# Kernel optimization log

Measured on AMD Instinct MI355X. Metric: run time of the kernel, lower is better.

The kernel has to match this reference:

```python
import jax, jax.numpy as jnp
import numpy as np

EPS = 1e-5
B, D_ENT, D_REL = 1024, 400, 400
OUT, KW = 32, 9
N_ENT = 50000


def _bn(x, g, b, axes):
    # batch-norm with batch statistics (training-mode math), eps=1e-5
    mu = jnp.mean(x, axis=axes, keepdims=True)
    var = jnp.var(x, axis=axes, keepdims=True)
    return (x - mu) * jax.lax.rsqrt(var + EPS) * g + b


def setup_inputs() -> dict:
    key = jax.random.key(0)
    ks = jax.random.split(key, 6)
    return {
        "e1_emb": jax.random.normal(ks[0], (B, D_ENT), jnp.float32),
        "rel_emb": jax.random.normal(ks[1], (B, D_REL), jnp.float32),
        "all_ent_w": jax.random.normal(ks[2], (N_ENT, D_ENT), jnp.float32),
        "fc1_w": jax.random.normal(ks[3], (OUT * KW, D_REL), jnp.float32) * 0.05,
        "fc1_b": jnp.zeros((OUT * KW,), jnp.float32),
        "fc_w": jax.random.normal(ks[4], (D_ENT, (D_ENT - KW + 1) * OUT), jnp.float32) * 0.02,
        "fc_b": jnp.zeros((D_ENT,), jnp.float32),
        "bn0_g": jnp.ones((1,), jnp.float32),
        "bn0_b": jnp.zeros((1,), jnp.float32),
        "bn1_g": jnp.ones((OUT,), jnp.float32),
        "bn1_b": jnp.zeros((OUT,), jnp.float32),
        "bn2_g": jnp.ones((D_ENT,), jnp.float32),
        "bn2_b": jnp.zeros((D_ENT,), jnp.float32),
    }


def reference(e1_emb, rel_emb, all_ent_w, fc1_w, fc1_b, fc_w, fc_b,
              bn0_g, bn0_b, bn1_g, bn1_b, bn2_g, bn2_b):
    d = e1_emb.shape[1]
    L = d - KW + 1  # conv output width (kernel_h=1, in_channels=1)

    # bn0: BatchNorm2d(1) over view [B,1,1,d] -> stats over all elements
    x = _bn(e1_emb, bn0_g, bn0_b, axes=(0, 1))  # [B, d]

    # hypernetwork: relation -> per-sample conv kernels [B, OUT, KW]
    k = (rel_emb @ fc1_w.T + fc1_b).reshape(-1, OUT, KW)

    # per-sample 1x9 conv (groups=B) as windows + batched contraction
    # xw[b, l, w] = x[b, l + w]
    xw = jnp.stack([x[:, w:w + L] for w in range(KW)], axis=-1)  # [B, L, KW]
    conv = jnp.einsum('blw,bow->bol', xw, k)  # [B, OUT, L]

    # bn1: BatchNorm2d(OUT), per-channel stats over (batch, width)
    h = _bn(conv, bn1_g[None, :, None], bn1_b[None, :, None], axes=(0, 2))

    # flatten channel-major (matches torch .view(B, -1) on [B, OUT, 1, L])
    h = h.reshape(h.shape[0], OUT * L)
    h = h @ fc_w.T + fc_b  # [B, d]

    # bn2: BatchNorm1d(d), per-feature stats over batch
    h = jax.nn.relu(_bn(h, bn2_g, bn2_b, axes=(0,)))

    return h @ all_ent_w.T  # [B, N_ENT]
```

## Files before the change

kernel.cpp:

```cpp
#include <hip/hip_runtime.h>
#include <stdint.h>

typedef unsigned short u16;
typedef short bf16x8 __attribute__((ext_vector_type(8)));
typedef float f32x4 __attribute__((ext_vector_type(4)));
typedef u16 u16x4 __attribute__((ext_vector_type(4)));
typedef u16 u16x8 __attribute__((ext_vector_type(8)));

#define B_SZ   1024
#define D_IN   400
#define L_OUT  392
#define OC     32
#define KW     9
#define K_FC   12544
#define N_ENT  50000
#define NPAD_ENT 50048
#define KPAD_H 448
#define NPAD_FC 512
#define SPLIT_FC 14

__device__ __forceinline__ u16 f2bf(float f) {
  uint32_t u = __builtin_bit_cast(uint32_t, f);
  u += 0x7FFFu + ((u >> 16) & 1u);
  return (u16)(u >> 16);
}
__device__ __forceinline__ float bf2f(u16 v) {
  uint32_t u = ((uint32_t)v) << 16;
  return __builtin_bit_cast(float, u);
}

__device__ __forceinline__ void gload_lds16(const u16* g, u16* l) {
  __builtin_amdgcn_global_load_lds(
      (const __attribute__((address_space(1))) unsigned int*)g,
      (__attribute__((address_space(3))) unsigned int*)l, 16, 0, 0);
}

__device__ __forceinline__ void block_reduce2(float& s1, float& s2, float* sm) {
  for (int d = 32; d; d >>= 1) { s1 += __shfl_down(s1, d); s2 += __shfl_down(s2, d); }
  int wave = threadIdx.x >> 6, lane = threadIdx.x & 63;
  if (lane == 0) { sm[wave * 2] = s1; sm[wave * 2 + 1] = s2; }
  __syncthreads();
  if (threadIdx.x == 0) {
    s1 = sm[0] + sm[2] + sm[4] + sm[6];
    s2 = sm[1] + sm[3] + sm[5] + sm[7];
  }
}

__global__ __launch_bounds__(256) void red0(const float* __restrict__ e1, float* __restrict__ part0) {
  int t = threadIdx.x;
  int idx = blockIdx.x * 256 + t;
  float s1 = 0.f, s2 = 0.f;
  for (int i = idx; i < B_SZ * D_IN; i += 256 * 256) { float v = e1[i]; s1 += v; s2 += v * v; }
  __shared__ float sm[8];
  block_reduce2(s1, s2, sm);
  if (t == 0) { part0[blockIdx.x * 2] = s1; part0[blockIdx.x * 2 + 1] = s2; }
}

__global__ __launch_bounds__(256) void comb0(const float* __restrict__ part0,
                                             const float* __restrict__ g0,
                                             const float* __restrict__ b0,
                                             float* __restrict__ stats) {
  int t = threadIdx.x;
  float s1 = part0[t * 2], s2 = part0[t * 2 + 1];
  __shared__ float sm[8];
  block_reduce2(s1, s2, sm);
  if (t == 0) {
    const float N = (float)(B_SZ * D_IN);
    float mu = s1 / N, var = s2 / N - mu * mu;
    float a = g0[0] * rsqrtf(var + 1e-5f);
    stats[0] = a;
    stats[1] = b0[0] - mu * a;
  }
}

__global__ __launch_bounds__(256) void fc1_gemm(const float* __restrict__ rel,
                                                const float* __restrict__ W,
                                                const float* __restrict__ bias,
                                                float* __restrict__ outk) {
  __shared__ __align__(16) float As[16 * 68];
  __shared__ __align__(16) float Bs[16 * 68];
  int mt = blockIdx.x, nt = blockIdx.y;
  int t = threadIdx.x;
  int tx = t & 15, ty = t >> 4;
  int lr = t >> 2, lk = (t & 3) * 4;
  float acc[4][4] = {};
  for (int k0 = 0; k0 < 400; k0 += 16) {
    __syncthreads();
    float4 av = *(const float4*)(rel + (size_t)(mt * 64 + lr) * 400 + k0 + lk);
    int brow = nt * 64 + lr;
    float4 bv = {0.f, 0.f, 0.f, 0.f};
    if (brow < 288) bv = *(const float4*)(W + (size_t)brow * 400 + k0 + lk);
    As[(lk + 0) * 68 + lr] = av.x; As[(lk + 1) * 68 + lr] = av.y;
    As[(lk + 2) * 68 + lr] = av.z; As[(lk + 3) * 68 + lr] = av.w;
    Bs[(lk + 0) * 68 + lr] = bv.x; Bs[(lk + 1) * 68 + lr] = bv.y;
    Bs[(lk + 2) * 68 + lr] = bv.z; Bs[(lk + 3) * 68 + lr] = bv.w;
    __syncthreads();
#pragma unroll
    for (int k = 0; k < 16; ++k) {
      float4 a = *(const float4*)(As + k * 68 + ty * 4);
      float4 b = *(const float4*)(Bs + k * 68 + tx * 4);
      float aa[4] = {a.x, a.y, a.z, a.w}, bb[4] = {b.x, b.y, b.z, b.w};
#pragma unroll
      for (int i = 0; i < 4; ++i)
#pragma unroll
        for (int j = 0; j < 4; ++j) acc[i][j] += aa[i] * bb[j];
    }
  }
#pragma unroll
  for (int i = 0; i < 4; ++i) {
    int row = mt * 64 + ty * 4 + i;
#pragma unroll
    for (int j = 0; j < 4; ++j) {
      int col = nt * 64 + tx * 4 + j;
      if (col < 288) outk[(size_t)row * 288 + col] = acc[i][j] + bias[col];
    }
  }
}

__global__ __launch_bounds__(256) void conv_kernel(const float* __restrict__ e1,
                                                   const float* __restrict__ stats,
                                                   const float* __restrict__ kbuf,
                                                   u16* __restrict__ convA,
                                                   float* __restrict__ partial1) {
  int b = blockIdx.x, t = threadIdx.x;
  __shared__ __align__(16) float xs[D_IN];
  __shared__ float ks[OC * KW];
  float a0 = stats[0], b0c = stats[1];
  for (int i = t; i < D_IN; i += 256) xs[i] = e1[(size_t)b * D_IN + i] * a0 + b0c;
  for (int i = t; i < OC * KW; i += 256) ks[i] = kbuf[(size_t)b * (OC * KW) + i];
  __syncthreads();
  int o = t >> 3, sub = t & 7;
  float kw[KW];
#pragma unroll
  for (int w = 0; w < KW; ++w) kw[w] = ks[o * KW + w];
  float s1 = 0.f, s2 = 0.f;
  u16* orow = convA + (size_t)b * K_FC + o * L_OUT;
#pragma unroll
  for (int it = 0; it < 13; ++it) {
    int l = sub * 4 + it * 32;
    if (l < L_OUT) {
      float4 x0 = *(const float4*)(xs + l);
      float4 x1 = *(const float4*)(xs + l + 4);
      float4 x2 = *(const float4*)(xs + l + 8);
      float xv[12] = {x0.x, x0.y, x0.z, x0.w, x1.x, x1.y, x1.z, x1.w, x2.x, x2.y, x2.z, x2.w};
      u16x4 st;
#pragma unroll
      for (int j = 0; j < 4; ++j) {
        float c = 0.f;
#pragma unroll
        for (int w = 0; w < KW; ++w) c += xv[j + w] * kw[w];
        s1 += c; s2 += c * c;
        st[j] = f2bf(c);
      }
      *(u16x4*)(orow + l) = st;
    }
  }
  s1 += __shfl_down(s1, 4); s2 += __shfl_down(s2, 4);
  s1 += __shfl_down(s1, 2); s2 += __shfl_down(s2, 2);
  s1 += __shfl_down(s1, 1); s2 += __shfl_down(s2, 1);
  if (sub == 0) {
    partial1[b * 64 + o] = s1;
    partial1[b * 64 + 32 + o] = s2;
  }
}

__global__ __launch_bounds__(256) void comb1(const float* __restrict__ partial1,
                                             const float* __restrict__ g1,
                                             float* __restrict__ alphaK) {
  __shared__ float red[256];
  __shared__ float ab[32];
  int t = threadIdx.x;
  int s = t & 63, q = t >> 6;
  float acc = 0.f;
  for (int b = q * 256; b < q * 256 + 256; ++b) acc += partial1[b * 64 + s];
  red[t] = acc;
  __syncthreads();
  if (t < 64) red[t] = red[t] + red[t + 64] + red[t + 128] + red[t + 192];
  __syncthreads();
  if (t < 32) {
    const float N = (float)(B_SZ * L_OUT);
    float S1 = red[t], S2 = red[t + 32];
    float mu = S1 / N, var = S2 / N - mu * mu;
    ab[t] = g1[t] * rsqrtf(var + 1e-5f);
  }
  __syncthreads();
  for (int i = t; i < K_FC; i += 256) {
    int o = i / L_OUT;
    alphaK[i] = ab[o];
  }
}

__global__ __launch_bounds__(256) void cvt_fcw(const float* __restrict__ src,
                                               const float* __restrict__ alphaK,
                                               u16* __restrict__ dst) {
  int gid = blockIdx.x * 256 + threadIdx.x;
  int row = gid / 1568, c = gid - row * 1568;
  int k = c * 8;
  u16x8 o = {};
  if (row < 400) {
    float4 f0 = *(const float4*)(src + (size_t)row * K_FC + k);
    float4 f1 = *(const float4*)(src + (size_t)row * K_FC + k + 4);
    float4 a0 = *(const float4*)(alphaK + k);
    float4 a1 = *(const float4*)(alphaK + k + 4);
    o[0] = f2bf(f0.x * a0.x); o[1] = f2bf(f0.y * a0.y);
    o[2] = f2bf(f0.z * a0.z); o[3] = f2bf(f0.w * a0.w);
    o[4] = f2bf(f1.x * a1.x); o[5] = f2bf(f1.y * a1.y);
    o[6] = f2bf(f1.z * a1.z); o[7] = f2bf(f1.w * a1.w);
  }
  *(u16x8*)(dst + (size_t)row * K_FC + k) = o;
}

__global__ __launch_bounds__(256) void cvt_ent(const float* __restrict__ src, u16* __restrict__ dst) {
  int gid = blockIdx.x * 256 + threadIdx.x;
  int row = gid / 56, c = gid - row * 56;
  int k = c * 8;
  u16x8 o = {};
  if (row < N_ENT && k < D_IN) {
    float4 f0 = *(const float4*)(src + (size_t)row * D_IN + k);
    float4 f1 = *(const float4*)(src + (size_t)row * D_IN + k + 4);
    o[0] = f2bf(f0.x); o[1] = f2bf(f0.y); o[2] = f2bf(f0.z); o[3] = f2bf(f0.w);
    o[4] = f2bf(f1.x); o[5] = f2bf(f1.y); o[6] = f2bf(f1.z); o[7] = f2bf(f1.w);
  }
  *(u16x8*)(dst + (size_t)row * KPAD_H + k) = o;
}

__global__ __launch_bounds__(256) void bn2_kernel(const float* __restrict__ part2,
                                                  const float* __restrict__ g2,
                                                  const float* __restrict__ b2,
                                                  u16* __restrict__ hfin) {
  int j0 = blockIdx.x * 16;
  int t = threadIdx.x;
  int tj = t & 15, tb = t >> 4;
  int j = j0 + tj;
  float v[64];
  float s1 = 0.f, s2 = 0.f;
#pragma unroll 2
  for (int i = 0; i < 64; ++i) {
    int b = tb + i * 16;
    float acc = 0.f;
#pragma unroll
    for (int s = 0; s < SPLIT_FC; ++s)
      acc += part2[((size_t)s * B_SZ + b) * NPAD_FC + j];
    v[i] = acc; s1 += acc; s2 += acc * acc;
  }
  __shared__ float sm1[16][17], sm2[16][17];
  sm1[tb][tj] = s1; sm2[tb][tj] = s2;
  __syncthreads();
  __shared__ float albe[2][16];
  if (t < 16) {
    float S1 = 0.f, S2 = 0.f;
#pragma unroll
    for (int r = 0; r < 16; ++r) { S1 += sm1[r][t]; S2 += sm2[r][t]; }
    int jf = j0 + t;
    float al = 0.f, be = 0.f;
    if (jf < D_IN) {
      float mu = S1 / 1024.f, var = S2 / 1024.f - mu * mu;
      al = g2[jf] * rsqrtf(var + 1e-5f);
      be = b2[jf] - mu * al;
    }
    albe[0][t] = al; albe[1][t] = be;
  }
  __syncthreads();
  float al = albe[0][tj], be = albe[1][tj];
#pragma unroll 2
  for (int i = 0; i < 64; ++i) {
    int b = tb + i * 16;
    hfin[(size_t)b * KPAD_H + j] = f2bf(fmaxf(v[i] * al + be, 0.f));
  }
}

__global__ __launch_bounds__(256) void gemm_bt(const u16* __restrict__ A,
                                               const u16* __restrict__ Bm,
                                               float* __restrict__ C,
                                               int Kpad, int mtiles, int ntiles,
                                               int ksteps_total, int ksteps_chunk,
                                               long ldc, int ncols_valid, long csplit_stride,
                                               int xcd_swz) {
  __shared__ __align__(16) u16 As[128 * 64];
  __shared__ __align__(16) u16 Bs[128 * 64];
  int bid = blockIdx.x;
  int mt, nt, sp;
  if (xcd_swz) {
    int r = bid & 7, g = bid >> 3;
    mt = g & 7;
    nt = (g >> 3) * 8 + r;
    sp = 0;
    if (nt >= ntiles) return;
  } else {
    mt = bid % mtiles;
    nt = (bid / mtiles) % ntiles;
    sp = bid / (mtiles * ntiles);
  }
  int kbeg = sp * ksteps_chunk;
  int kend = kbeg + ksteps_chunk;
  if (kend > ksteps_total) kend = ksteps_total;

  int tid = threadIdx.x;
  int wave = tid >> 6, lane = tid & 63;
  int quad = lane >> 4, m16 = lane & 15;
  int rbase = (wave >> 1) * 64, cbase = (wave & 1) * 64;

  const u16* Arow0 = A + (size_t)mt * 128 * Kpad;
  const u16* Brow0 = Bm + (size_t)nt * 128 * Kpad;

  f32x4 acc[4][4] = {};

  for (int kt = kbeg; kt < kend; ++kt) {
    int k0 = kt * 64;
    __syncthreads();
#pragma unroll
    for (int p = 0; p < 4; ++p) {
      int slin = p * 256 + tid;
      int row = slin >> 3;
      int gch = (slin & 7) ^ (row & 7);
      u16* la = As + ((p * 256 + (wave << 6)) << 3);
      u16* lb = Bs + ((p * 256 + (wave << 6)) << 3);
      gload_lds16(Arow0 + (size_t)row * Kpad + k0 + gch * 8, la);
      gload_lds16(Brow0 + (size_t)row * Kpad + k0 + gch * 8, lb);
    }
    __syncthreads();
#pragma unroll
    for (int s = 0; s < 2; ++s) {
      bf16x8 af[4], bfr[4];
#pragma unroll
      for (int i = 0; i < 4; ++i) {
        int ar = rbase + i * 16 + m16;
        af[i] = *(const bf16x8*)(As + ar * 64 + (((s * 4 + quad) ^ (ar & 7)) << 3));
        int bc = cbase + i * 16 + m16;
        bfr[i] = *(const bf16x8*)(Bs + bc * 64 + (((s * 4 + quad) ^ (bc & 7)) << 3));
      }
#pragma unroll
      for (int i = 0; i < 4; ++i)
#pragma unroll
        for (int j = 0; j < 4; ++j)
          acc[i][j] = __builtin_amdgcn_mfma_f32_16x16x32_bf16(af[i], bfr[j], acc[i][j], 0, 0, 0);
    }
  }

  float* Cb = C + (size_t)sp * csplit_stride;
#pragma unroll
  for (int i = 0; i < 4; ++i) {
#pragma unroll
    for (int j = 0; j < 4; ++j) {
      int col = nt * 128 + cbase + j * 16 + m16;
      if (col < ncols_valid) {
        int row0 = mt * 128 + rbase + i * 16 + quad * 4;
#pragma unroll
        for (int r = 0; r < 4; ++r)
          Cb[(size_t)(row0 + r) * ldc + col] = acc[i][j][r];
      }
    }
  }
}

extern "C" void kernel_launch(void* const* d_in, const int* in_sizes, int n_in,
                              void* d_out, int out_size, void* d_ws, size_t ws_size,
                              hipStream_t stream) {
  const float* e1   = (const float*)d_in[0];
  const float* rel  = (const float*)d_in[1];
  const float* entw = (const float*)d_in[2];
  const float* fc1w = (const float*)d_in[3];
  const float* fc1b = (const float*)d_in[4];
  const float* fcw  = (const float*)d_in[5];
  const float* bn0g = (const float*)d_in[7];
  const float* bn0b = (const float*)d_in[8];
  const float* bn1g = (const float*)d_in[9];
  const float* bn2g = (const float*)d_in[11];
  const float* bn2b = (const float*)d_in[12];
  float* out = (float*)d_out;

  char* ws = (char*)d_ws;
  size_t off = 0;
  auto alloc = [&](size_t bytes) -> void* {
    off = (off + 255) & ~(size_t)255;
    void* p = ws + off;
    off += bytes;
    return p;
  };
  float* stats    = (float*)alloc(16 * 4);
  float* part0    = (float*)alloc(512 * 4);
  float* kbuf     = (float*)alloc((size_t)B_SZ * 288 * 4);
  float* partial1 = (float*)alloc((size_t)B_SZ * 64 * 4);
  float* alphaK   = (float*)alloc((size_t)K_FC * 4);
  u16*   convA    = (u16*)alloc((size_t)B_SZ * K_FC * 2);
  u16*   fcwb     = (u16*)alloc((size_t)NPAD_FC * K_FC * 2);
  float* part2    = (float*)alloc((size_t)SPLIT_FC * B_SZ * NPAD_FC * 4);
  u16*   hfin     = (u16*)alloc((size_t)B_SZ * KPAD_H * 2);
  u16*   entb     = (u16*)alloc((size_t)NPAD_ENT * KPAD_H * 2);

  red0<<<256, 256, 0, stream>>>(e1, part0);
  comb0<<<1, 256, 0, stream>>>(part0, bn0g, bn0b, stats);
  fc1_gemm<<<dim3(16, 5), 256, 0, stream>>>(rel, fc1w, fc1b, kbuf);
  conv_kernel<<<B_SZ, 256, 0, stream>>>(e1, stats, kbuf, convA, partial1);
  comb1<<<1, 256, 0, stream>>>(partial1, bn1g, alphaK);
  cvt_fcw<<<3136, 256, 0, stream>>>(fcw, alphaK, fcwb);
  gemm_bt<<<8 * 4 * SPLIT_FC, 256, 0, stream>>>(convA, fcwb, part2, K_FC, 8, 4, 196, 14,
                                                (long)NPAD_FC, NPAD_FC, (long)B_SZ * NPAD_FC, 0);
  bn2_kernel<<<KPAD_H / 16, 256, 0, stream>>>(part2, bn2g, bn2b, hfin);
  cvt_ent<<<10948, 256, 0, stream>>>(entw, entb);
  gemm_bt<<<8 * 392, 256, 0, stream>>>(hfin, entb, out, KPAD_H, 8, 391, 7, 7,
                                       (long)N_ENT, N_ENT, 0, 1);
}
```

Before: 557.0 us.

## Fuse entity weight bf16 conversion into final GEMM and fold comb0 into fc1

The separate cvt_ent pass and the entb workspace are removed. The final GEMM now reads fp32 entity weights directly, converts them to bf16 in registers and stores them into swizzled LDS tiles, while the activation tile still arrives through global-to-LDS loads. This avoids writing and rereading about 45 MB of bf16 weights. The cost is that each entity tile is read once per M tile (8 times) as fp32, which the L2 cache may or may not absorb. Separately, the bn0 statistics combine step moves into block (0,0) of fc1_gemm, saving one kernel launch.

```diff
diff --git a/kernel.cpp b/kernel.cpp
--- a/kernel.cpp
+++ b/kernel.cpp
@@ -14,7 +14,6 @@
 #define KW     9
 #define K_FC   12544
 #define N_ENT  50000
-#define NPAD_ENT 50048
 #define KPAD_H 448
 #define NPAD_FC 512
 #define SPLIT_FC 14
@@ -56,29 +55,17 @@
   if (t == 0) { part0[blockIdx.x * 2] = s1; part0[blockIdx.x * 2 + 1] = s2; }
 }
 
-__global__ __launch_bounds__(256) void comb0(const float* __restrict__ part0,
-                                             const float* __restrict__ g0,
-                                             const float* __restrict__ b0,
-                                             float* __restrict__ stats) {
-  int t = threadIdx.x;
-  float s1 = part0[t * 2], s2 = part0[t * 2 + 1];
-  __shared__ float sm[8];
-  block_reduce2(s1, s2, sm);
-  if (t == 0) {
-    const float N = (float)(B_SZ * D_IN);
-    float mu = s1 / N, var = s2 / N - mu * mu;
-    float a = g0[0] * rsqrtf(var + 1e-5f);
-    stats[0] = a;
-    stats[1] = b0[0] - mu * a;
-  }
-}
-
 __global__ __launch_bounds__(256) void fc1_gemm(const float* __restrict__ rel,
                                                 const float* __restrict__ W,
                                                 const float* __restrict__ bias,
-                                                float* __restrict__ outk) {
+                                                float* __restrict__ outk,
+                                                const float* __restrict__ part0,
+                                                const float* __restrict__ g0,
+                                                const float* __restrict__ b0,
+                                                float* __restrict__ stats) {
   __shared__ __align__(16) float As[16 * 68];
   __shared__ __align__(16) float Bs[16 * 68];
+  __shared__ float sm0[8];
   int mt = blockIdx.x, nt = blockIdx.y;
   int t = threadIdx.x;
   int tx = t & 15, ty = t >> 4;
@@ -113,6 +100,18 @@
     for (int j = 0; j < 4; ++j) {
       int col = nt * 64 + tx * 4 + j;
       if (col < 288) outk[(size_t)row * 288 + col] = acc[i][j] + bias[col];
+    }
+  }
+  if (mt == 0 && nt == 0) {
+    float s1 = part0[t * 2], s2 = part0[t * 2 + 1];
+    __syncthreads();
+    block_reduce2(s1, s2, sm0);
+    if (t == 0) {
+      const float N = (float)(B_SZ * D_IN);
+      float mu = s1 / N, var = s2 / N - mu * mu;
+      float a = g0[0] * rsqrtf(var + 1e-5f);
+      stats[0] = a;
+      stats[1] = b0[0] - mu * a;
     }
   }
 }
@@ -210,20 +209,6 @@
   *(u16x8*)(dst + (size_t)row * K_FC + k) = o;
 }
 
-__global__ __launch_bounds__(256) void cvt_ent(const float* __restrict__ src, u16* __restrict__ dst) {
-  int gid = blockIdx.x * 256 + threadIdx.x;
-  int row = gid / 56, c = gid - row * 56;
-  int k = c * 8;
-  u16x8 o = {};
-  if (row < N_ENT && k < D_IN) {
-    float4 f0 = *(const float4*)(src + (size_t)row * D_IN + k);
-    float4 f1 = *(const float4*)(src + (size_t)row * D_IN + k + 4);
-    o[0] = f2bf(f0.x); o[1] = f2bf(f0.y); o[2] = f2bf(f0.z); o[3] = f2bf(f0.w);
-    o[4] = f2bf(f1.x); o[5] = f2bf(f1.y); o[6] = f2bf(f1.z); o[7] = f2bf(f1.w);
-  }
-  *(u16x8*)(dst + (size_t)row * KPAD_H + k) = o;
-}
-
 __global__ __launch_bounds__(256) void bn2_kernel(const float* __restrict__ part2,
                                                   const float* __restrict__ g2,
                                                   const float* __restrict__ b2,
@@ -274,23 +259,13 @@
                                                float* __restrict__ C,
                                                int Kpad, int mtiles, int ntiles,
                                                int ksteps_total, int ksteps_chunk,
-                                               long ldc, int ncols_valid, long csplit_stride,
-                                               int xcd_swz) {
+                                               long ldc, int ncols_valid, long csplit_stride) {
   __shared__ __align__(16) u16 As[128 * 64];
   __shared__ __align__(16) u16 Bs[128 * 64];
   int bid = blockIdx.x;
-  int mt, nt, sp;
-  if (xcd_swz) {
-    int r = bid & 7, g = bid >> 3;
-    mt = g & 7;
-    nt = (g >> 3) * 8 + r;
-    sp = 0;
-    if (nt >= ntiles) return;
-  } else {
-    mt = bid % mtiles;
-    nt = (bid / mtiles) % ntiles;
-    sp = bid / (mtiles * ntiles);
-  }
+  int mt = bid % mtiles;
+  int nt = (bid / mtiles) % ntiles;
+  int sp = bid / (mtiles * ntiles);
   int kbeg = sp * ksteps_chunk;
   int kend = kbeg + ksteps_chunk;
   if (kend > ksteps_total) kend = ksteps_total;
@@ -348,6 +323,97 @@
 #pragma unroll
         for (int r = 0; r < 4; ++r)
           Cb[(size_t)(row0 + r) * ldc + col] = acc[i][j][r];
+      }
+    }
+  }
+}
+
+__global__ __launch_bounds__(256) void gemm_ent(const u16* __restrict__ A,
+                                                const float* __restrict__ Bf,
+                                                float* __restrict__ C) {
+  __shared__ __align__(16) u16 As[128 * 64];
+  __shared__ __align__(16) u16 Bs[128 * 64];
+  int bid = blockIdx.x;
+  int r = bid & 7, g = bid >> 3;
+  int mt = g & 7;
+  int nt = (g >> 3) * 8 + r;
+  if (nt >= 391) return;
+
+  int tid = threadIdx.x;
+  int wave = tid >> 6, lane = tid & 63;
+  int quad = lane >> 4, m16 = lane & 15;
+  int rbase = (wave >> 1) * 64, cbase = (wave & 1) * 64;
+
+  const u16* Arow0 = A + (size_t)mt * 128 * KPAD_H;
+
+  f32x4 acc[4][4] = {};
+
+  for (int kt = 0; kt < 7; ++kt) {
+    int k0 = kt * 64;
+    __syncthreads();
+    float4 fb[4][2];
+#pragma unroll
+    for (int p = 0; p < 4; ++p) {
+      int slin = p * 256 + tid;
+      int row = slin >> 3;
+      int gch = (slin & 7) ^ (row & 7);
+      int gr = nt * 128 + row;
+      int gk = k0 + gch * 8;
+      if (gr < N_ENT && gk < D_IN) {
+        fb[p][0] = *(const float4*)(Bf + (size_t)gr * D_IN + gk);
+        fb[p][1] = *(const float4*)(Bf + (size_t)gr * D_IN + gk + 4);
+      } else {
+        fb[p][0] = float4{0.f, 0.f, 0.f, 0.f};
+        fb[p][1] = float4{0.f, 0.f, 0.f, 0.f};
+      }
+    }
+#pragma unroll
+    for (int p = 0; p < 4; ++p) {
+      int slin = p * 256 + tid;
+      int row = slin >> 3;
+      int gch = (slin & 7) ^ (row & 7);
+      u16* la = As + ((p * 256 + (wave << 6)) << 3);
+      gload_lds16(Arow0 + (size_t)row * KPAD_H + k0 + gch * 8, la);
+    }
+#pragma unroll
+    for (int p = 0; p < 4; ++p) {
+      int slin = p * 256 + tid;
+      u16x8 st;
+      st[0] = f2bf(fb[p][0].x); st[1] = f2bf(fb[p][0].y);
+      st[2] = f2bf(fb[p][0].z); st[3] = f2bf(fb[p][0].w);
+      st[4] = f2bf(fb[p][1].x); st[5] = f2bf(fb[p][1].y);
+      st[6] = f2bf(fb[p][1].z); st[7] = f2bf(fb[p][1].w);
+      *(u16x8*)(Bs + slin * 8) = st;
+    }
+    __syncthreads();
+#pragma unroll
+    for (int s = 0; s < 2; ++s) {
+      bf16x8 af[4], bfr[4];
+#pragma unroll
+      for (int i = 0; i < 4; ++i) {
+        int ar = rbase + i * 16 + m16;
+        af[i] = *(const bf16x8*)(As + ar * 64 + (((s * 4 + quad) ^ (ar & 7)) << 3));
+        int bc = cbase + i * 16 + m16;
+        bfr[i] = *(const bf16x8*)(Bs + bc * 64 + (((s * 4 + quad) ^ (bc & 7)) << 3));
+      }
+#pragma unroll
+      for (int i = 0; i < 4; ++i)
+#pragma unroll
+        for (int j = 0; j < 4; ++j)
+          acc[i][j] = __builtin_amdgcn_mfma_f32_16x16x32_bf16(af[i], bfr[j], acc[i][j], 0, 0, 0);
+    }
+  }
+
+#pragma unroll
+  for (int i = 0; i < 4; ++i) {
+#pragma unroll
+    for (int j = 0; j < 4; ++j) {
+      int col = nt * 128 + cbase + j * 16 + m16;
+      if (col < N_ENT) {
+        int row0 = mt * 128 + rbase + i * 16 + quad * 4;
+#pragma unroll
+        for (int r = 0; r < 4; ++r)
+          C[(size_t)(row0 + r) * N_ENT + col] = acc[i][j][r];
       }
     }
   }
@@ -386,18 +452,14 @@
   u16*   fcwb     = (u16*)alloc((size_t)NPAD_FC * K_FC * 2);
   float* part2    = (float*)alloc((size_t)SPLIT_FC * B_SZ * NPAD_FC * 4);
   u16*   hfin     = (u16*)alloc((size_t)B_SZ * KPAD_H * 2);
-  u16*   entb     = (u16*)alloc((size_t)NPAD_ENT * KPAD_H * 2);
 
   red0<<<256, 256, 0, stream>>>(e1, part0);
-  comb0<<<1, 256, 0, stream>>>(part0, bn0g, bn0b, stats);
-  fc1_gemm<<<dim3(16, 5), 256, 0, stream>>>(rel, fc1w, fc1b, kbuf);
+  fc1_gemm<<<dim3(16, 5), 256, 0, stream>>>(rel, fc1w, fc1b, kbuf, part0, bn0g, bn0b, stats);
   conv_kernel<<<B_SZ, 256, 0, stream>>>(e1, stats, kbuf, convA, partial1);
   comb1<<<1, 256, 0, stream>>>(partial1, bn1g, alphaK);
   cvt_fcw<<<3136, 256, 0, stream>>>(fcw, alphaK, fcwb);
   gemm_bt<<<8 * 4 * SPLIT_FC, 256, 0, stream>>>(convA, fcwb, part2, K_FC, 8, 4, 196, 14,
-                                                (long)NPAD_FC, NPAD_FC, (long)B_SZ * NPAD_FC, 0);
+                                                (long)NPAD_FC, NPAD_FC, (long)B_SZ * NPAD_FC);
   bn2_kernel<<<KPAD_H / 16, 256, 0, stream>>>(part2, bn2g, bn2b, hfin);
-  cvt_ent<<<10948, 256, 0, stream>>>(entw, entb);
-  gemm_bt<<<8 * 392, 256, 0, stream>>>(hfin, entb, out, KPAD_H, 8, 391, 7, 7,
-                                       (long)N_ENT, N_ENT, 0, 1);
-}
+  gemm_ent<<<8 * 392, 256, 0, stream>>>(hfin, entw, out);
+}
```

New measurement: 563.8 us. About the same (+1.2%).
